# Optimization experiments

Measured on AMD Instinct MI355X. Metric: run time of the kernel, lower is better.

The kernel has to match this reference:

```python
import jax, jax.numpy as jnp
import numpy as np

B, I, O = 2048, 512, 512

def setup_inputs() -> dict:
    key = jax.random.key(0)
    kx, kw, ks = jax.random.split(key, 3)
    x = jax.random.uniform(kx, (B, I), dtype=jnp.float32)
    # shift weight logits so sigmoid(w) ~ 0.02: keeps the length-I product
    # of implication factors away from underflow (sparse conjunction)
    w_logits = jax.random.normal(kw, (I, O), dtype=jnp.float32) - 4.0
    s_logits = jax.random.normal(ks, (I, O), dtype=jnp.float32)
    return {"x": x, "w_logits": w_logits, "s_logits": s_logits}

def reference(x, w_logits, s_logits):
    # FuzzyParam.value(): sigmoid of stored logits
    w = jax.nn.sigmoid(w_logits)   # (I, O)
    s = jax.nn.sigmoid(s_logits)   # (I, O)
    xi = x[:, :, None]             # (B, I, 1)
    # product fuzzy logic:
    #   bin_xnor(a, b) = a*b + (1-a)*(1-b)
    #   implies(a, b)  = 1 - a*(1 - b)
    #   conjoin        = prod along axis
    xnor = xi * s + (1.0 - xi) * (1.0 - s)      # (B, I, O)
    factors = 1.0 - w * (1.0 - xnor)            # (B, I, O)
    return jnp.prod(factors, axis=1)            # (B, O)
```

## Files before the change

kernel.cpp:

```cpp
#include <hip/hip_runtime.h>
#include <math.h>

#define B_DIM 2048
#define I_DIM 512
#define O_DIM 512

constexpr int R_ROWS  = 16;
constexpr int W_CHUNK = 4;
constexpr int CHUNK   = I_DIM / W_CHUNK;
constexpr int KP      = CHUNK / 2;


__global__ __launch_bounds__(256) void setup_kernel(
    const float* __restrict__ w_logits,
    const float* __restrict__ s_logits,
    float4* __restrict__ ab4)
{
    int t  = blockIdx.x * 256 + threadIdx.x;
    int o  = t & (O_DIM - 1);
    int k  = t >> 9;
    int i0 = 2 * k;

    float zw0 = w_logits[(i0 + 0) * O_DIM + o];
    float zs0 = s_logits[(i0 + 0) * O_DIM + o];
    float zw1 = w_logits[(i0 + 1) * O_DIM + o];
    float zs1 = s_logits[(i0 + 1) * O_DIM + o];

    float w0 = 1.0f / (1.0f + expf(-zw0));
    float s0 = 1.0f / (1.0f + expf(-zs0));
    float w1 = 1.0f / (1.0f + expf(-zw1));
    float s1 = 1.0f / (1.0f + expf(-zs1));

    float4 v;
    v.x = fmaf(-w0, s0, 1.0f);
    v.y = fmaf(-w1, s1, 1.0f);
    v.z = w0 * (2.0f * s0 - 1.0f);
    v.w = w1 * (2.0f * s1 - 1.0f);
    ab4[k * O_DIM + o] = v;
}

__global__ __launch_bounds__(1024, 4) void fuzzy_main(
    const float* __restrict__ x,
    const float4* __restrict__ ab4,
    float* __restrict__ out)
{
    __shared__ __align__(16) unsigned char sh_raw[W_CHUNK * R_ROWS * 256 * 4];
    float4 (*xs4)[CHUNK]        = reinterpret_cast<float4(*)[CHUNK]>(sh_raw);
    float  (*part)[R_ROWS][256] = reinterpret_cast<float(*)[R_ROWS][256]>(sh_raw);

    const int o_l = threadIdx.x;
    const int o   = blockIdx.x * 256 + o_l;
    const int y   = __builtin_amdgcn_readfirstlane((int)threadIdx.y);
    const int g   = blockIdx.y;
    const int b0  = g * R_ROWS;
    const int kbase = y * KP;

    const float4* ab_o = ab4 + o;

    float4 pA0 = ab_o[(size_t)(kbase + 0) * O_DIM];
    float4 pA1 = ab_o[(size_t)(kbase + 1) * O_DIM];
    float4 pB0 = ab_o[(size_t)(kbase + 2) * O_DIM];
    float4 pB1 = ab_o[(size_t)(kbase + 3) * O_DIM];

    {
        const float4* x4 = (const float4*)x;
        const int tid = threadIdx.y * 256 + o_l;
#pragma unroll
        for (int p = 0; p < 2; ++p) {
            int fidx = p * 1024 + tid;
            int r = fidx >> 7;
            int q = fidx & (CHUNK - 1);
            xs4[r][q] = x4[(size_t)(b0 + r) * (I_DIM / 4) + q];
        }
    }
    __syncthreads();

    float acc[R_ROWS];
#pragma unroll
    for (int r = 0; r < R_ROWS; ++r) acc[r] = 1.0f;

    for (int k = 0; k < KP; k += 4) {
        const int qA = (kbase + k) >> 1;
        {
            float4 c0 = pA0, c1 = pA1;
            pA0 = ab_o[(size_t)(kbase + k + 4) * O_DIM];
            pA1 = ab_o[(size_t)(kbase + k + 5) * O_DIM];
#pragma unroll
            for (int r = 0; r < R_ROWS; ++r) {
                float4 xv = xs4[r][qA];
                float f0 = fmaf(c0.z, xv.x, c0.x);
                float f1 = fmaf(c0.w, xv.y, c0.y);
                float f2 = fmaf(c1.z, xv.z, c1.x);
                float f3 = fmaf(c1.w, xv.w, c1.y);
                acc[r] *= (f0 * f2) * (f1 * f3);
            }
        }
        {
            float4 c0 = pB0, c1 = pB1;
            pB0 = ab_o[(size_t)(kbase + k + 6) * O_DIM];
            pB1 = ab_o[(size_t)(kbase + k + 7) * O_DIM];
#pragma unroll
            for (int r = 0; r < R_ROWS; ++r) {
                float4 xv = xs4[r][qA + 1];
                float f0 = fmaf(c0.z, xv.x, c0.x);
                float f1 = fmaf(c0.w, xv.y, c0.y);
                float f2 = fmaf(c1.z, xv.z, c1.x);
                float f3 = fmaf(c1.w, xv.w, c1.y);
                acc[r] *= (f0 * f2) * (f1 * f3);
            }
        }
    }

    __syncthreads();
#pragma unroll
    for (int r = 0; r < R_ROWS; ++r)
        part[y][r][o_l] = acc[r];
    __syncthreads();
#pragma unroll
    for (int rr = 0; rr < 4; ++rr) {
        int r = y * 4 + rr;
        float v = part[0][r][o_l] * part[1][r][o_l]
                * part[2][r][o_l] * part[3][r][o_l];
        out[(size_t)(b0 + r) * O_DIM + o] = v;
    }
}

extern "C" void kernel_launch(void* const* d_in, const int* in_sizes, int n_in,
                              void* d_out, int out_size, void* d_ws, size_t ws_size,
                              hipStream_t stream) {
    const float* x        = (const float*)d_in[0];
    const float* w_logits = (const float*)d_in[1];
    const float* s_logits = (const float*)d_in[2];
    float* out = (float*)d_out;
    float4* ab4 = (float4*)d_ws;

    setup_kernel<<<dim3(512), dim3(256), 0, stream>>>(w_logits, s_logits, ab4);

    fuzzy_main<<<dim3(O_DIM / 256, B_DIM / R_ROWS), dim3(256, W_CHUNK), 0, stream>>>(
        x, ab4, out);
}
```

Before: 97.91 us.

## Register-tile four outputs per thread and split I across eight waves

```diff
diff --git a/kernel.cpp b/kernel.cpp
--- a/kernel.cpp
+++ b/kernel.cpp
@@ -6,10 +6,12 @@
 #define O_DIM 512
 
 constexpr int R_ROWS  = 16;
-constexpr int W_CHUNK = 4;
+constexpr int T_O     = 4;
+constexpr int LANES   = 64;
+constexpr int W_CHUNK = 8;
+constexpr int O_BLK   = LANES * T_O;
 constexpr int CHUNK   = I_DIM / W_CHUNK;
-constexpr int KP      = CHUNK / 2;
-
+constexpr int QPT     = CHUNK / 4;
 
 __global__ __launch_bounds__(256) void setup_kernel(
     const float* __restrict__ w_logits,
@@ -39,89 +41,126 @@
     ab4[k * O_DIM + o] = v;
 }
 
-__global__ __launch_bounds__(1024, 4) void fuzzy_main(
+__global__ __launch_bounds__(512, 2) void fuzzy_main(
     const float* __restrict__ x,
     const float4* __restrict__ ab4,
     float* __restrict__ out)
 {
-    __shared__ __align__(16) unsigned char sh_raw[W_CHUNK * R_ROWS * 256 * 4];
-    float4 (*xs4)[CHUNK]        = reinterpret_cast<float4(*)[CHUNK]>(sh_raw);
-    float  (*part)[R_ROWS][256] = reinterpret_cast<float(*)[R_ROWS][256]>(sh_raw);
+    __shared__ __align__(16) unsigned char sh_raw[4 * R_ROWS * O_BLK * 4];
+    float4 (*xs4)[I_DIM / 4] =
+        reinterpret_cast<float4(*)[I_DIM / 4]>(sh_raw);
+    float (*part)[R_ROWS][O_BLK] =
+        reinterpret_cast<float(*)[R_ROWS][O_BLK]>(sh_raw);
 
-    const int o_l = threadIdx.x;
-    const int o   = blockIdx.x * 256 + o_l;
-    const int y   = __builtin_amdgcn_readfirstlane((int)threadIdx.y);
-    const int g   = blockIdx.y;
-    const int b0  = g * R_ROWS;
-    const int kbase = y * KP;
+    const int lane  = threadIdx.x;
+    const int y     = __builtin_amdgcn_readfirstlane((int)threadIdx.y);
+    const int tid   = y * LANES + lane;
+    const int obase = blockIdx.x * O_BLK;
+    const int g     = blockIdx.y;
+    const int b0    = g * R_ROWS;
+    const int qbase = y * QPT;
 
-    const float4* ab_o = ab4 + o;
+    const float4* abp = ab4 + obase + lane;
 
-    float4 pA0 = ab_o[(size_t)(kbase + 0) * O_DIM];
-    float4 pA1 = ab_o[(size_t)(kbase + 1) * O_DIM];
-    float4 pB0 = ab_o[(size_t)(kbase + 2) * O_DIM];
-    float4 pB1 = ab_o[(size_t)(kbase + 3) * O_DIM];
+    float4 cA0[T_O], cA1[T_O], cB0[T_O], cB1[T_O];
+#pragma unroll
+    for (int j = 0; j < T_O; ++j) {
+        cA0[j] = abp[(size_t)(2 * qbase + 0) * O_DIM + 64 * j];
+        cA1[j] = abp[(size_t)(2 * qbase + 1) * O_DIM + 64 * j];
+        cB0[j] = abp[(size_t)(2 * qbase + 2) * O_DIM + 64 * j];
+        cB1[j] = abp[(size_t)(2 * qbase + 3) * O_DIM + 64 * j];
+    }
 
     {
         const float4* x4 = (const float4*)x;
-        const int tid = threadIdx.y * 256 + o_l;
 #pragma unroll
-        for (int p = 0; p < 2; ++p) {
-            int fidx = p * 1024 + tid;
+        for (int p = 0; p < 4; ++p) {
+            int fidx = p * 512 + tid;
             int r = fidx >> 7;
-            int q = fidx & (CHUNK - 1);
+            int q = fidx & 127;
             xs4[r][q] = x4[(size_t)(b0 + r) * (I_DIM / 4) + q];
         }
     }
     __syncthreads();
 
-    float acc[R_ROWS];
+    float acc[R_ROWS][T_O];
 #pragma unroll
-    for (int r = 0; r < R_ROWS; ++r) acc[r] = 1.0f;
+    for (int r = 0; r < R_ROWS; ++r)
+#pragma unroll
+        for (int j = 0; j < T_O; ++j) acc[r][j] = 1.0f;
 
-    for (int k = 0; k < KP; k += 4) {
-        const int qA = (kbase + k) >> 1;
+    for (int qq = 0; qq < QPT; qq += 2) {
         {
-            float4 c0 = pA0, c1 = pA1;
-            pA0 = ab_o[(size_t)(kbase + k + 4) * O_DIM];
-            pA1 = ab_o[(size_t)(kbase + k + 5) * O_DIM];
+            const int q = qbase + qq;
+            float4 xv[R_ROWS];
+#pragma unroll
+            for (int r = 0; r < R_ROWS; ++r) xv[r] = xs4[r][q];
 #pragma unroll
             for (int r = 0; r < R_ROWS; ++r) {
-                float4 xv = xs4[r][qA];
-                float f0 = fmaf(c0.z, xv.x, c0.x);
-                float f1 = fmaf(c0.w, xv.y, c0.y);
-                float f2 = fmaf(c1.z, xv.z, c1.x);
-                float f3 = fmaf(c1.w, xv.w, c1.y);
-                acc[r] *= (f0 * f2) * (f1 * f3);
+#pragma unroll
+                for (int j = 0; j < T_O; ++j) {
+                    float f0 = fmaf(cA0[j].z, xv[r].x, cA0[j].x);
+                    float f1 = fmaf(cA0[j].w, xv[r].y, cA0[j].y);
+                    float f2 = fmaf(cA1[j].z, xv[r].z, cA1[j].x);
+                    float f3 = fmaf(cA1[j].w, xv[r].w, cA1[j].y);
+                    acc[r][j] *= (f0 * f2) * (f1 * f3);
+                }
+            }
+#pragma unroll
+            for (int j = 0; j < T_O; ++j) {
+                cA0[j] = abp[(size_t)(2 * q + 4) * O_DIM + 64 * j];
+                cA1[j] = abp[(size_t)(2 * q + 5) * O_DIM + 64 * j];
             }
         }
         {
-            float4 c0 = pB0, c1 = pB1;
-            pB0 = ab_o[(size_t)(kbase + k + 6) * O_DIM];
-            pB1 = ab_o[(size_t)(kbase + k + 7) * O_DIM];
+            const int q = qbase + qq + 1;
+            float4 xv[R_ROWS];
+#pragma unroll
+            for (int r = 0; r < R_ROWS; ++r) xv[r] = xs4[r][q];
 #pragma unroll
             for (int r = 0; r < R_ROWS; ++r) {
-                float4 xv = xs4[r][qA + 1];
-                float f0 = fmaf(c0.z, xv.x, c0.x);
-                float f1 = fmaf(c0.w, xv.y, c0.y);
-                float f2 = fmaf(c1.z, xv.z, c1.x);
-                float f3 = fmaf(c1.w, xv.w, c1.y);
-                acc[r] *= (f0 * f2) * (f1 * f3);
+#pragma unroll
+                for (int j = 0; j < T_O; ++j) {
+                    float f0 = fmaf(cB0[j].z, xv[r].x, cB0[j].x);
+                    float f1 = fmaf(cB0[j].w, xv[r].y, cB0[j].y);
+                    float f2 = fmaf(cB1[j].z, xv[r].z, cB1[j].x);
+                    float f3 = fmaf(cB1[j].w, xv[r].w, cB1[j].y);
+                    acc[r][j] *= (f0 * f2) * (f1 * f3);
+                }
+            }
+#pragma unroll
+            for (int j = 0; j < T_O; ++j) {
+                cB0[j] = abp[(size_t)(2 * q + 4) * O_DIM + 64 * j];
+                cB1[j] = abp[(size_t)(2 * q + 5) * O_DIM + 64 * j];
             }
         }
     }
 
     __syncthreads();
+    if (y < 4) {
 #pragma unroll
-    for (int r = 0; r < R_ROWS; ++r)
-        part[y][r][o_l] = acc[r];
+        for (int r = 0; r < R_ROWS; ++r)
+#pragma unroll
+            for (int j = 0; j < T_O; ++j)
+                part[y][r][64 * j + lane] = acc[r][j];
+    }
+    __syncthreads();
+    if (y >= 4) {
+#pragma unroll
+        for (int r = 0; r < R_ROWS; ++r)
+#pragma unroll
+            for (int j = 0; j < T_O; ++j)
+                part[y - 4][r][64 * j + lane] *= acc[r][j];
+    }
     __syncthreads();
 #pragma unroll
-    for (int rr = 0; rr < 4; ++rr) {
-        int r = y * 4 + rr;
-        float v = part[0][r][o_l] * part[1][r][o_l]
-                * part[2][r][o_l] * part[3][r][o_l];
-        out[(size_t)(b0 + r) * O_DIM + o] = v;
+    for (int p = 0; p < 8; ++p) {
+        int idx = p * 512 + tid;
+        int r = idx >> 8;
+        int c = idx & (O_BLK - 1);
+        float v = part[0][r][c] * part[1][r][c]
+                * part[2][r][c] * part[3][r][c];
+        out[(size_t)(b0 + r) * O_DIM + obase + c] = v;
     }
 }
 
@@ -136,6 +175,6 @@
 
     setup_kernel<<<dim3(512), dim3(256), 0, stream>>>(w_logits, s_logits, ab4);
 
-    fuzzy_main<<<dim3(O_DIM / 256, B_DIM / R_ROWS), dim3(256, W_CHUNK), 0, stream>>>(
+    fuzzy_main<<<dim3(O_DIM / O_BLK, B_DIM / R_ROWS), dim3(LANES, W_CHUNK), 0, stream>>>(
         x, ab4, out);
 }
```

New measurement: 128.6 us. +31.3%, slower.

## Remap work so lanes own batch rows and coefficients are wave-uniform

Applied to the files above, without the earlier changes.

```diff
diff --git a/kernel.cpp b/kernel.cpp
--- a/kernel.cpp
+++ b/kernel.cpp
@@ -5,21 +5,21 @@
 #define I_DIM 512
 #define O_DIM 512
 
-constexpr int R_ROWS  = 16;
-constexpr int W_CHUNK = 4;
-constexpr int CHUNK   = I_DIM / W_CHUNK;
-constexpr int KP      = CHUNK / 2;
-
+constexpr int LANES = 64;
+constexpr int T_O   = 8;
+constexpr int NW    = 8;
+constexpr int C_I   = 64;
+constexpr int QPC2  = C_I / 4;
 
 __global__ __launch_bounds__(256) void setup_kernel(
     const float* __restrict__ w_logits,
     const float* __restrict__ s_logits,
-    float4* __restrict__ ab4)
+    float4* __restrict__ abT)
 {
-    int t  = blockIdx.x * 256 + threadIdx.x;
-    int o  = t & (O_DIM - 1);
-    int k  = t >> 9;
-    int i0 = 2 * k;
+    const int tid = threadIdx.x;
+    const int k   = blockIdx.x >> 1;
+    const int o   = (blockIdx.x & 1) * 256 + tid;
+    const int i0  = 2 * k;
 
     float zw0 = w_logits[(i0 + 0) * O_DIM + o];
     float zs0 = s_logits[(i0 + 0) * O_DIM + o];
@@ -36,92 +36,63 @@
     v.y = fmaf(-w1, s1, 1.0f);
     v.z = w0 * (2.0f * s0 - 1.0f);
     v.w = w1 * (2.0f * s1 - 1.0f);
-    ab4[k * O_DIM + o] = v;
+    abT[(size_t)o * 256 + k] = v;
 }
 
-__global__ __launch_bounds__(1024, 4) void fuzzy_main(
+__global__ __launch_bounds__(512, 2) void fuzzy_main(
     const float* __restrict__ x,
-    const float4* __restrict__ ab4,
+    const float4* __restrict__ abT,
     float* __restrict__ out)
 {
-    __shared__ __align__(16) unsigned char sh_raw[W_CHUNK * R_ROWS * 256 * 4];
-    float4 (*xs4)[CHUNK]        = reinterpret_cast<float4(*)[CHUNK]>(sh_raw);
-    float  (*part)[R_ROWS][256] = reinterpret_cast<float(*)[R_ROWS][256]>(sh_raw);
+    __shared__ float part[NW][LANES][T_O + 1];
 
-    const int o_l = threadIdx.x;
-    const int o   = blockIdx.x * 256 + o_l;
-    const int y   = __builtin_amdgcn_readfirstlane((int)threadIdx.y);
-    const int g   = blockIdx.y;
-    const int b0  = g * R_ROWS;
-    const int kbase = y * KP;
+    const int lane = threadIdx.x;
+    const int y    = __builtin_amdgcn_readfirstlane((int)threadIdx.y);
+    const int bid  = blockIdx.x;
+    const int o0   = (bid & 63) * T_O;
+    const int b0   = (bid >> 6) * LANES;
 
-    const float4* ab_o = ab4 + o;
+    const float4* xp = (const float4*)x
+                     + (size_t)(b0 + lane) * (I_DIM / 4) + y * QPC2;
+    float4 xv[QPC2];
+#pragma unroll
+    for (int t = 0; t < QPC2; ++t) xv[t] = xp[t];
 
-    float4 pA0 = ab_o[(size_t)(kbase + 0) * O_DIM];
-    float4 pA1 = ab_o[(size_t)(kbase + 1) * O_DIM];
-    float4 pB0 = ab_o[(size_t)(kbase + 2) * O_DIM];
-    float4 pB1 = ab_o[(size_t)(kbase + 3) * O_DIM];
+    const int kbase = y * (C_I / 2);
+    const float4* ab0 = abT + (size_t)o0 * 256 + kbase;
 
-    {
-        const float4* x4 = (const float4*)x;
-        const int tid = threadIdx.y * 256 + o_l;
+    float acc[T_O];
 #pragma unroll
-        for (int p = 0; p < 2; ++p) {
-            int fidx = p * 1024 + tid;
-            int r = fidx >> 7;
-            int q = fidx & (CHUNK - 1);
-            xs4[r][q] = x4[(size_t)(b0 + r) * (I_DIM / 4) + q];
-        }
-    }
-    __syncthreads();
+    for (int j = 0; j < T_O; ++j) acc[j] = 1.0f;
 
-    float acc[R_ROWS];
 #pragma unroll
-    for (int r = 0; r < R_ROWS; ++r) acc[r] = 1.0f;
-
-    for (int k = 0; k < KP; k += 4) {
-        const int qA = (kbase + k) >> 1;
-        {
-            float4 c0 = pA0, c1 = pA1;
-            pA0 = ab_o[(size_t)(kbase + k + 4) * O_DIM];
-            pA1 = ab_o[(size_t)(kbase + k + 5) * O_DIM];
+    for (int q = 0; q < QPC2; ++q) {
+        float4 xq = xv[q];
 #pragma unroll
-            for (int r = 0; r < R_ROWS; ++r) {
-                float4 xv = xs4[r][qA];
-                float f0 = fmaf(c0.z, xv.x, c0.x);
-                float f1 = fmaf(c0.w, xv.y, c0.y);
-                float f2 = fmaf(c1.z, xv.z, c1.x);
-                float f3 = fmaf(c1.w, xv.w, c1.y);
-                acc[r] *= (f0 * f2) * (f1 * f3);
-            }
-        }
-        {
-            float4 c0 = pB0, c1 = pB1;
-            pB0 = ab_o[(size_t)(kbase + k + 6) * O_DIM];
-            pB1 = ab_o[(size_t)(kbase + k + 7) * O_DIM];
-#pragma unroll
-            for (int r = 0; r < R_ROWS; ++r) {
-                float4 xv = xs4[r][qA + 1];
-                float f0 = fmaf(c0.z, xv.x, c0.x);
-                float f1 = fmaf(c0.w, xv.y, c0.y);
-                float f2 = fmaf(c1.z, xv.z, c1.x);
-                float f3 = fmaf(c1.w, xv.w, c1.y);
-                acc[r] *= (f0 * f2) * (f1 * f3);
-            }
+        for (int j = 0; j < T_O; ++j) {
+            float4 e0 = ab0[j * 256 + 2 * q];
+            float4 e1 = ab0[j * 256 + 2 * q + 1];
+            float f0 = fmaf(e0.z, xq.x, e0.x);
+            float f1 = fmaf(e0.w, xq.y, e0.y);
+            float f2 = fmaf(e1.z, xq.z, e1.x);
+            float f3 = fmaf(e1.w, xq.w, e1.y);
+            acc[j] *= (f0 * f2) * (f1 * f3);
         }
     }
 
+#pragma unroll
+    for (int j = 0; j < T_O; ++j)
+        part[y][lane][j] = acc[j];
     __syncthreads();
-#pragma unroll
-    for (int r = 0; r < R_ROWS; ++r)
-        part[y][r][o_l] = acc[r];
-    __syncthreads();
-#pragma unroll
-    for (int rr = 0; rr < 4; ++rr) {
-        int r = y * 4 + rr;
-        float v = part[0][r][o_l] * part[1][r][o_l]
-                * part[2][r][o_l] * part[3][r][o_l];
-        out[(size_t)(b0 + r) * O_DIM + o] = v;
+    {
+        const int tid = y * LANES + lane;
+        const int b   = tid >> 3;
+        const int j   = tid & 7;
+        float v = ((part[0][b][j] * part[1][b][j])
+                 * (part[2][b][j] * part[3][b][j]))
+                * ((part[4][b][j] * part[5][b][j])
+                 * (part[6][b][j] * part[7][b][j]));
+        out[(size_t)(b0 + b) * O_DIM + o0 + j] = v;
     }
 }
 
@@ -132,10 +103,9 @@
     const float* w_logits = (const float*)d_in[1];
     const float* s_logits = (const float*)d_in[2];
     float* out = (float*)d_out;
-    float4* ab4 = (float4*)d_ws;
+    float4* abT = (float4*)d_ws;
 
-    setup_kernel<<<dim3(512), dim3(256), 0, stream>>>(w_logits, s_logits, ab4);
+    setup_kernel<<<dim3(512), dim3(256), 0, stream>>>(w_logits, s_logits, abT);
 
-    fuzzy_main<<<dim3(O_DIM / 256, B_DIM / R_ROWS), dim3(256, W_CHUNK), 0, stream>>>(
-        x, ab4, out);
+    fuzzy_main<<<dim3(2048), dim3(LANES, NW), 0, stream>>>(x, abT, out);
 }
```

After: 123.1 us. +25.7%, slower.
